# Kernel optimization log

Measured on AMD Instinct MI355X. Metric: run time of the kernel, lower is better.

The kernel has to match this reference:

```python
import jax, jax.numpy as jnp
import numpy as np


def setup_inputs() -> dict:
    key = jax.random.key(0)
    ks = jax.random.split(key, 8)
    B, T, F, H, O = 512, 128, 512, 512, 256
    s = 0.05
    return {
        "states": jax.random.normal(ks[0], (B, T, F), jnp.float32),
        "terminated": jax.random.bernoulli(ks[1], 0.02, (B, T)),
        "h0": jnp.zeros((B, H), jnp.float32),
        "W_ih": jax.random.normal(ks[2], (H, F), jnp.float32) * s,
        "W_hh": jax.random.normal(ks[3], (H, H), jnp.float32) * s,
        "b_ih": jax.random.normal(ks[4], (H,), jnp.float32) * s,
        "b_hh": jax.random.normal(ks[5], (H,), jnp.float32) * s,
        "fc_w": jax.random.normal(ks[6], (O, H), jnp.float32) * s,
        "fc_b": jax.random.normal(ks[7], (O,), jnp.float32) * s,
    }


def reference(states, terminated, h0, W_ih, W_hh, b_ih, b_hh, fc_w, fc_b):
    # states: [B, T, F]; terminated: [B, T] bool; h0: [B, H] (num_layers=1)
    B, T, F = states.shape
    # Precompute the input projection once (big GEMM outside the scan).
    x_proj = jnp.einsum("btf,hf->bth", states, W_ih) + b_ih + b_hh  # [B, T, H]
    x_proj_t = jnp.swapaxes(x_proj, 0, 1)          # [T, B, H]
    term_t = jnp.swapaxes(terminated, 0, 1)        # [T, B]

    def step(h, inp):
        xp, tm = inp                               # xp: [B, H], tm: [B]
        h_new = jnp.tanh(xp + h @ W_hh.T)          # vanilla RNN (tanh) cell
        # Zero hidden state of envs that terminated at this step (applied
        # AFTER emitting the output, matching the torch segment-reset logic).
        h_next = jnp.where(tm[:, None], jnp.zeros_like(h_new), h_new)
        return h_next, h_new

    h_final, outs = jax.lax.scan(step, h0, (x_proj_t, term_t))  # outs: [T, B, H]
    rnn_output = jnp.swapaxes(outs, 0, 1).reshape(B * T, -1)    # [B*T, H]
    logits = rnn_output @ fc_w.T + fc_b                          # [B*T, O]
    return logits, h_final
```

## Files before the change

### kernel.cpp

```cpp
#include <hip/hip_runtime.h>
#include <hip/hip_bf16.h>
#include <hip/hip_fp16.h>


typedef _Float16 half8 __attribute__((ext_vector_type(8)));
typedef _Float16 half4 __attribute__((ext_vector_type(4)));
typedef float f32x4 __attribute__((ext_vector_type(4)));

#define XPW_OFF   0UL
#define WIH_OFF   67108864UL
#define FCW_OFF   67633152UL
#define BIAS_OFF  67895296UL
#define WRESA_OFF 67897344UL
#define WRESL_OFF 68290560UL


#define HB_STRIDE 136

#define LDS_BARRIER()                                              \
    do {                                                           \
        __builtin_amdgcn_sched_barrier(0);                         \
        asm volatile("s_waitcnt lgkmcnt(0)" ::: "memory");         \
        __builtin_amdgcn_s_barrier();                              \
        __builtin_amdgcn_sched_barrier(0);                         \
    } while (0)

__global__ void conv_w(const float* __restrict__ Wih, const float* __restrict__ Whh,
                       const float* __restrict__ fcw, const float* __restrict__ bih,
                       const float* __restrict__ bhh,
                       _Float16* __restrict__ wih_h, _Float16* __restrict__ fcw_h,
                       float* __restrict__ bias2,
                       _Float16* __restrict__ wresA, _Float16* __restrict__ wresL) {
    int idx = blockIdx.x * 256 + threadIdx.x;
    if (idx < 262144) wih_h[idx] = (_Float16)Wih[idx];
    if (idx < 196608) {
        const int i = idx & 7, l = (idx >> 3) & 63, s = (idx >> 9) & 15;
        const int rest = idx >> 13;
        const int w = rest / 3, nt = rest % 3;
        const int row = w * 64 + (l & 15) * 4 + nt;
        wresA[idx] = (_Float16)Whh[(size_t)row * 512 + s * 32 + (l >> 4) * 8 + i];
    }
    if (idx < 65536) {
        const int i = idx & 7, l = (idx >> 3) & 63, s = (idx >> 9) & 15, w = idx >> 13;
        const int row = w * 64 + (l & 15) * 4 + 3;
        wresL[idx] = (_Float16)Whh[(size_t)row * 512 + s * 32 + (l >> 4) * 8 + i];
    }
    if (idx < 131072) fcw_h[idx] = (_Float16)fcw[idx];
    if (idx < 512) bias2[idx] = bih[idx] + bhh[idx];
}

__global__ __launch_bounds__(256) void gemm_xproj(const float* __restrict__ A,
                                                  const _Float16* __restrict__ Bw,
                                                  const float* __restrict__ bias2,
                                                  _Float16* __restrict__ out) {
    __shared__ _Float16 As[128 * 32];
    __shared__ _Float16 Bs[128 * 32];
    __shared__ _Float16 ep[128 * 128];
    const int tid = threadIdx.x;
    const int s_ = blockIdx.x;
    const int z = s_ & 7, k_ = s_ >> 3;
    const int gid = z * 256 + k_;
    const int b = gid >> 2;
    const int cb2 = gid & 3;
    const int lane = tid & 63, w1 = tid >> 6;
    const int wr = (w1 >> 1) * 64, wc = (w1 & 1) * 64;
    const int ln = lane & 15, kg = lane >> 4;

    f32x4 acc[4][4];
#pragma unroll
    for (int m = 0; m < 4; m++)
#pragma unroll
        for (int n = 0; n < 4; n++) acc[m][n] = (f32x4)0.0f;

    const int sr = tid >> 1, sc = (tid & 1) * 16;
    const int brow = cb2 * 128 + sr;

    for (int k0 = 0; k0 < 512; k0 += 32) {
        {
            const float* ga = A + (size_t)(b * 128 + sr) * 512 + k0 + sc;
            float4 f0 = *(const float4*)(ga + 0);
            float4 f1 = *(const float4*)(ga + 4);
            float4 f2 = *(const float4*)(ga + 8);
            float4 f3 = *(const float4*)(ga + 12);
            half8 h0, h1;
            h0[0] = (_Float16)f0.x; h0[1] = (_Float16)f0.y; h0[2] = (_Float16)f0.z; h0[3] = (_Float16)f0.w;
            h0[4] = (_Float16)f1.x; h0[5] = (_Float16)f1.y; h0[6] = (_Float16)f1.z; h0[7] = (_Float16)f1.w;
            h1[0] = (_Float16)f2.x; h1[1] = (_Float16)f2.y; h1[2] = (_Float16)f2.z; h1[3] = (_Float16)f2.w;
            h1[4] = (_Float16)f3.x; h1[5] = (_Float16)f3.y; h1[6] = (_Float16)f3.z; h1[7] = (_Float16)f3.w;
            *(half8*)&As[sr * 32 + sc] = h0;
            *(half8*)&As[sr * 32 + sc + 8] = h1;
        }
        {
            const _Float16* gb = Bw + (size_t)brow * 512 + k0 + sc;
            *(half8*)&Bs[sr * 32 + sc] = *(const half8*)(gb);
            *(half8*)&Bs[sr * 32 + sc + 8] = *(const half8*)(gb + 8);
        }
        __syncthreads();
        half8 af[4], bf[4];
#pragma unroll
        for (int m = 0; m < 4; m++) af[m] = *(const half8*)&As[(wr + m * 16 + ln) * 32 + kg * 8];
#pragma unroll
        for (int n = 0; n < 4; n++) bf[n] = *(const half8*)&Bs[(wc + n * 16 + ln) * 32 + kg * 8];
#pragma unroll
        for (int m = 0; m < 4; m++)
#pragma unroll
            for (int n = 0; n < 4; n++)
                acc[m][n] = __builtin_amdgcn_mfma_f32_16x16x32_f16(af[m], bf[n], acc[m][n], 0, 0, 0);
        __syncthreads();
    }
    float bv[4];
#pragma unroll
    for (int n = 0; n < 4; n++) bv[n] = bias2[cb2 * 128 + wc + n * 16 + ln];
#pragma unroll
    for (int m = 0; m < 4; m++)
#pragma unroll
        for (int q = 0; q < 4; q++) {
            const int t = wr + m * 16 + kg * 4 + q;
#pragma unroll
            for (int n = 0; n < 4; n++)
                ep[t * 128 + wc + n * 16 + ln] = (_Float16)(acc[m][n][q] + bv[n]);
        }
    __syncthreads();
    const int bg = b >> 4, kgs = (b >> 2) & 3, qs = b & 3;
    const size_t obase = (size_t)(bg * 128) * 8192 + (size_t)(cb2 * 2 * 64 + kgs * 16) * 16 + qs * 4;
#pragma unroll
    for (int j = 0; j < 16; j++) {
        const int wid = j * 256 + tid;
        const int t2 = wid >> 5, slb = wid & 31;
        const half4 v = *(const half4*)&ep[t2 * 128 + slb * 4];
        *(half4*)&out[obase + (size_t)t2 * 8192 + (slb >> 4) * 1024 + (slb & 15) * 16] = v;
    }
}

__global__ __launch_bounds__(512, 2) void rnn_scan16(
    const _Float16* __restrict__ xps,
    const _Float16* __restrict__ wresA,
    const _Float16* __restrict__ wresL,
    const int* __restrict__ term,
    const float* __restrict__ h0,
    float* dout) {
    __shared__ __align__(16) _Float16 hb[64 * HB_STRIDE];
    __shared__ __align__(16) _Float16 wl[65536];
    __shared__ unsigned int term_lds[16][4];
    const int tid = threadIdx.x;
    const int bg = blockIdx.x;
    const int R0 = bg * 16;
    const int lane = tid & 63, w = tid >> 6;
    const int ln = lane & 15, kg = lane >> 4;
    _Float16* rnn = (_Float16*)dout;

    half8 wf[48];
    {
        const _Float16* wp = wresA + (size_t)w * 24576 + lane * 8;
#pragma unroll
        for (int f = 0; f < 48; f++) wf[f] = *(const half8*)(wp + (size_t)f * 512);
    }
#pragma unroll
    for (int f = 0; f < 48; f++) asm volatile("" : "+a"(wf[f]));

    for (int u = 0; u < 16; u++) {
        const int o = (u * 512 + tid) * 8;
        *(half8*)&wl[o] = *(const half8*)(wresL + o);
    }
    {
        const int r = tid >> 5, c0 = (tid & 31) * 16;
        const float* gh = h0 + (size_t)(R0 + r) * 512 + c0;
        half8 v0, v1;
#pragma unroll
        for (int i = 0; i < 8; i++) { v0[i] = (_Float16)gh[i]; v1[i] = (_Float16)gh[8 + i]; }
        const int kb = c0 >> 3;
        *(half8*)&hb[kb * HB_STRIDE + r * 8] = v0;
        *(half8*)&hb[(kb + 1) * HB_STRIDE + r * 8] = v1;
    }
    if (tid < 64) {
        const int r = tid >> 2, word = tid & 3;
        unsigned int m = 0;
        for (int b2 = 0; b2 < 32; b2++)
            m |= (term[(R0 + r) * 128 + word * 32 + b2] ? 1u : 0u) << b2;
        term_lds[r][word] = m;
    }
    __syncthreads();

    const _Float16* xpt = xps + (size_t)(bg * 128) * 8192 + tid * 16;
    const _Float16* bl = &wl[(size_t)w * 8192];
    const int cb = w * 64 + ln * 4;
    const int hoff = (cb >> 3) * HB_STRIDE + (cb & 7);
    unsigned int tmask[4];

#pragma unroll 1
    for (int t = 0; t < 128; ++t) {
        if ((t & 31) == 0) {
#pragma unroll
            for (int q = 0; q < 4; q++) tmask[q] = term_lds[kg * 4 + q][t >> 5];
        }
        const half8 xv0 = *(const half8*)(xpt);
        const half8 xv1 = *(const half8*)(xpt + 8);
        xpt += 8192;

        f32x4 acc[4];
#pragma unroll
        for (int n = 0; n < 4; n++) acc[n] = (f32x4)0.0f;

#pragma unroll
        for (int s = 0; s < 16; s++) {
            const half8 a = *(const half8*)&hb[(s * 4 + kg) * HB_STRIDE + ln * 8];
            acc[0] = __builtin_amdgcn_mfma_f32_16x16x32_f16(a, wf[s],      acc[0], 0, 0, 0);
            acc[1] = __builtin_amdgcn_mfma_f32_16x16x32_f16(a, wf[16 + s], acc[1], 0, 0, 0);
            acc[2] = __builtin_amdgcn_mfma_f32_16x16x32_f16(a, wf[32 + s], acc[2], 0, 0, 0);
            const half8 b4 = *(const half8*)(bl + s * 512 + lane * 8);
            acc[3] = __builtin_amdgcn_mfma_f32_16x16x32_f16(a, b4, acc[3], 0, 0, 0);
        }
        LDS_BARRIER();

        half4 hh4[4];
#pragma unroll
        for (int q = 0; q < 4; q++) {
            const bool dead = (tmask[q] >> (t & 31)) & 1;
            half4 v;
#pragma unroll
            for (int nt = 0; nt < 4; nt++) {
                const int u = q * 4 + nt;
                const float xval = (float)(u < 8 ? xv0[u] : xv1[u - 8]);
                const float pre = acc[nt][q] + xval;
                const float e = __expf(2.0f * pre);
                v[nt] = (_Float16)(1.0f - 2.0f * __builtin_amdgcn_rcpf(e + 1.0f));
            }
            hh4[q] = v;
            half4 mv = v;
            if (dead) { mv[0] = (_Float16)0; mv[1] = (_Float16)0; mv[2] = (_Float16)0; mv[3] = (_Float16)0; }
            *(half4*)&hb[hoff + (kg * 4 + q) * 8] = mv;
        }
        LDS_BARRIER();

#pragma unroll
        for (int q = 0; q < 4; q++)
            *(half4*)&rnn[((size_t)(R0 + kg * 4 + q) * 128 + t) * 512 + cb] = hh4[q];
    }

    {
        const int r = tid >> 5, c0 = (tid & 31) * 16;
        const int kb = c0 >> 3;
        half8 v0 = *(const half8*)&hb[kb * HB_STRIDE + r * 8];
        half8 v1 = *(const half8*)&hb[(kb + 1) * HB_STRIDE + r * 8];
        float* gf = dout + (size_t)65536 * 256 + (size_t)(R0 + r) * 512 + c0;
#pragma unroll
        for (int i = 0; i < 8; i++) { gf[i] = (float)v0[i]; gf[8 + i] = (float)v1[i]; }
    }
}

__global__ __launch_bounds__(512) void gemm_logits(const _Float16* Arnn,
                                                   const _Float16* __restrict__ Bw,
                                                   const float* __restrict__ biasv,
                                                   float* out) {
    __shared__ _Float16 As[128 * 32];
    __shared__ _Float16 Bs[256 * 32];
    const int tid = threadIdx.x;
    const int m0 = blockIdx.x * 128;
    const int lane = tid & 63, w = tid >> 6;
    const int wr = (w >> 2) * 64, wc = (w & 3) * 64;
    const int ln = lane & 15, kg = lane >> 4;

    f32x4 acc[4][4];
#pragma unroll
    for (int m = 0; m < 4; m++)
#pragma unroll
        for (int n = 0; n < 4; n++) acc[m][n] = (f32x4)0.0f;

    const int ar = tid >> 2, ac = (tid & 3) * 8;
    const int br = tid >> 1, bc = (tid & 1) * 16;

    for (int k0 = 0; k0 < 512; k0 += 32) {
        *(half8*)&As[ar * 32 + ac] = *(const half8*)(Arnn + (size_t)(m0 + ar) * 512 + k0 + ac);
        {
            const _Float16* gb = Bw + (size_t)br * 512 + k0 + bc;
            *(half8*)&Bs[br * 32 + bc] = *(const half8*)(gb);
            *(half8*)&Bs[br * 32 + bc + 8] = *(const half8*)(gb + 8);
        }
        __syncthreads();
        half8 af[4], bf[4];
#pragma unroll
        for (int m = 0; m < 4; m++) af[m] = *(const half8*)&As[(wr + m * 16 + ln) * 32 + kg * 8];
#pragma unroll
        for (int n = 0; n < 4; n++) bf[n] = *(const half8*)&Bs[(wc + n * 16 + ln) * 32 + kg * 8];
#pragma unroll
        for (int m = 0; m < 4; m++)
#pragma unroll
            for (int n = 0; n < 4; n++)
                acc[m][n] = __builtin_amdgcn_mfma_f32_16x16x32_f16(af[m], bf[n], acc[m][n], 0, 0, 0);
        __syncthreads();
    }
#pragma unroll
    for (int m = 0; m < 4; m++)
#pragma unroll
        for (int n = 0; n < 4; n++) {
            const int col = wc + n * 16 + ln;
            const float bv = biasv[col];
#pragma unroll
            for (int q = 0; q < 4; q++) {
                const int row = m0 + wr + m * 16 + kg * 4 + q;
                out[(size_t)row * 256 + col] = acc[m][n][q] + bv;
            }
        }
}

extern "C" void kernel_launch(void* const* d_in, const int* in_sizes, int n_in,
                              void* d_out, int out_size, void* d_ws, size_t ws_size,
                              hipStream_t stream) {
    const float* states = (const float*)d_in[0];
    const int*   term   = (const int*)d_in[1];
    const float* h0     = (const float*)d_in[2];
    const float* Wih    = (const float*)d_in[3];
    const float* Whh    = (const float*)d_in[4];
    const float* bih    = (const float*)d_in[5];
    const float* bhh    = (const float*)d_in[6];
    const float* fcw    = (const float*)d_in[7];
    const float* fcb    = (const float*)d_in[8];

    char* ws = (char*)d_ws;
    _Float16* xpw   = (_Float16*)(ws + XPW_OFF);
    _Float16* wih_h = (_Float16*)(ws + WIH_OFF);
    _Float16* fcw_h = (_Float16*)(ws + FCW_OFF);
    float*    bias2 = (float*)(ws + BIAS_OFF);
    _Float16* wresA = (_Float16*)(ws + WRESA_OFF);
    _Float16* wresL = (_Float16*)(ws + WRESL_OFF);

    conv_w<<<1024, 256, 0, stream>>>(Wih, Whh, fcw, bih, bhh, wih_h, fcw_h, bias2, wresA, wresL);
    gemm_xproj<<<2048, 256, 0, stream>>>(states, wih_h, bias2, xpw);
    rnn_scan16<<<32, 512, 0, stream>>>(xpw, wresA, wresL, term, h0, (float*)d_out);
    gemm_logits<<<512, 512, 0, stream>>>((const _Float16*)d_out, fcw_h, fcb, (float*)d_out);
}
```

Before: 397.3 us.

## Double-buffer RNN hidden state in LDS to drop one barrier per step

```diff
diff --git a/kernel.cpp b/kernel.cpp
--- a/kernel.cpp
+++ b/kernel.cpp
@@ -14,8 +14,6 @@
 #define WRESA_OFF 67897344UL
 #define WRESL_OFF 68290560UL
 
-
-#define HB_STRIDE 136
 
 #define LDS_BARRIER()                                              \
     do {                                                           \
@@ -132,16 +130,15 @@
     }
 }
 
-__global__ __launch_bounds__(512, 2) void rnn_scan16(
+__global__ __launch_bounds__(512, 2) void rnn_scan17(
     const _Float16* __restrict__ xps,
     const _Float16* __restrict__ wresA,
     const _Float16* __restrict__ wresL,
     const int* __restrict__ term,
     const float* __restrict__ h0,
     float* dout) {
-    __shared__ __align__(16) _Float16 hb[64 * HB_STRIDE];
+    __shared__ __align__(16) _Float16 hb[16384];
     __shared__ __align__(16) _Float16 wl[65536];
-    __shared__ unsigned int term_lds[16][4];
     const int tid = threadIdx.x;
     const int bg = blockIdx.x;
     const int R0 = bg * 16;
@@ -158,6 +155,28 @@
 #pragma unroll
     for (int f = 0; f < 48; f++) asm volatile("" : "+a"(wf[f]));
 
+    unsigned tmr0[4], tmr1[4], tmr2[4], tmr3[4];
+    {
+        unsigned* tw = (unsigned*)wl;
+        if (tid < 64) {
+            const int r = tid >> 2, word = tid & 3;
+            unsigned m = 0;
+            for (int b2 = 0; b2 < 32; b2++)
+                m |= (term[(R0 + r) * 128 + word * 32 + b2] ? 1u : 0u) << b2;
+            tw[tid] = m;
+        }
+        __syncthreads();
+#pragma unroll
+        for (int q = 0; q < 4; q++) {
+            const int r4 = (kg * 4 + q) * 4;
+            tmr0[q] = tw[r4 + 0];
+            tmr1[q] = tw[r4 + 1];
+            tmr2[q] = tw[r4 + 2];
+            tmr3[q] = tw[r4 + 3];
+        }
+        __syncthreads();
+    }
+
     for (int u = 0; u < 16; u++) {
         const int o = (u * 512 + tid) * 8;
         *(half8*)&wl[o] = *(const half8*)(wresL + o);
@@ -169,48 +188,51 @@
 #pragma unroll
         for (int i = 0; i < 8; i++) { v0[i] = (_Float16)gh[i]; v1[i] = (_Float16)gh[8 + i]; }
         const int kb = c0 >> 3;
-        *(half8*)&hb[kb * HB_STRIDE + r * 8] = v0;
-        *(half8*)&hb[(kb + 1) * HB_STRIDE + r * 8] = v1;
-    }
-    if (tid < 64) {
-        const int r = tid >> 2, word = tid & 3;
-        unsigned int m = 0;
-        for (int b2 = 0; b2 < 32; b2++)
-            m |= (term[(R0 + r) * 128 + word * 32 + b2] ? 1u : 0u) << b2;
-        term_lds[r][word] = m;
+        *(half8*)&hb[kb * 128 + ((r ^ (kb & 7)) << 3)] = v0;
+        *(half8*)&hb[(kb + 1) * 128 + ((r ^ ((kb + 1) & 7)) << 3)] = v1;
     }
     __syncthreads();
 
     const _Float16* xpt = xps + (size_t)(bg * 128) * 8192 + tid * 16;
     const _Float16* bl = &wl[(size_t)w * 8192];
     const int cb = w * 64 + ln * 4;
-    const int hoff = (cb >> 3) * HB_STRIDE + (cb & 7);
-    unsigned int tmask[4];
+    const int kbw = cb >> 3;
+    const int A0 = kg * 128 + ((ln ^ kg) << 3);
+    const int A1 = kg * 128 + ((ln ^ (kg + 4)) << 3);
+    int woff[4];
+#pragma unroll
+    for (int q = 0; q < 4; q++)
+        woff[q] = kbw * 128 + ((((kg * 4 + q) ^ (kbw & 7))) << 3) + (cb & 7);
+    unsigned tmask[4];
 
 #pragma unroll 1
     for (int t = 0; t < 128; ++t) {
         if ((t & 31) == 0) {
-#pragma unroll
-            for (int q = 0; q < 4; q++) tmask[q] = term_lds[kg * 4 + q][t >> 5];
+            const int sel = t >> 5;
+#pragma unroll
+            for (int q = 0; q < 4; q++)
+                tmask[q] = sel == 0 ? tmr0[q] : sel == 1 ? tmr1[q] : sel == 2 ? tmr2[q] : tmr3[q];
         }
         const half8 xv0 = *(const half8*)(xpt);
         const half8 xv1 = *(const half8*)(xpt + 8);
         xpt += 8192;
 
+        const _Float16* hr = hb + (t & 1) * 8192;
+        _Float16* hw = hb + ((t & 1) ^ 1) * 8192;
+
         f32x4 acc[4];
 #pragma unroll
         for (int n = 0; n < 4; n++) acc[n] = (f32x4)0.0f;
 
 #pragma unroll
         for (int s = 0; s < 16; s++) {
-            const half8 a = *(const half8*)&hb[(s * 4 + kg) * HB_STRIDE + ln * 8];
+            const half8 a = *(const half8*)&hr[s * 512 + ((s & 1) ? A1 : A0)];
             acc[0] = __builtin_amdgcn_mfma_f32_16x16x32_f16(a, wf[s],      acc[0], 0, 0, 0);
             acc[1] = __builtin_amdgcn_mfma_f32_16x16x32_f16(a, wf[16 + s], acc[1], 0, 0, 0);
             acc[2] = __builtin_amdgcn_mfma_f32_16x16x32_f16(a, wf[32 + s], acc[2], 0, 0, 0);
             const half8 b4 = *(const half8*)(bl + s * 512 + lane * 8);
             acc[3] = __builtin_amdgcn_mfma_f32_16x16x32_f16(a, b4, acc[3], 0, 0, 0);
         }
-        LDS_BARRIER();
 
         half4 hh4[4];
 #pragma unroll
@@ -228,20 +250,21 @@
             hh4[q] = v;
             half4 mv = v;
             if (dead) { mv[0] = (_Float16)0; mv[1] = (_Float16)0; mv[2] = (_Float16)0; mv[3] = (_Float16)0; }
-            *(half4*)&hb[hoff + (kg * 4 + q) * 8] = mv;
-        }
-        LDS_BARRIER();
+            *(half4*)&hw[woff[q]] = mv;
+        }
 
 #pragma unroll
         for (int q = 0; q < 4; q++)
             *(half4*)&rnn[((size_t)(R0 + kg * 4 + q) * 128 + t) * 512 + cb] = hh4[q];
+
+        LDS_BARRIER();
     }
 
     {
         const int r = tid >> 5, c0 = (tid & 31) * 16;
         const int kb = c0 >> 3;
-        half8 v0 = *(const half8*)&hb[kb * HB_STRIDE + r * 8];
-        half8 v1 = *(const half8*)&hb[(kb + 1) * HB_STRIDE + r * 8];
+        half8 v0 = *(const half8*)&hb[kb * 128 + ((r ^ (kb & 7)) << 3)];
+        half8 v1 = *(const half8*)&hb[(kb + 1) * 128 + ((r ^ ((kb + 1) & 7)) << 3)];
         float* gf = dout + (size_t)65536 * 256 + (size_t)(R0 + r) * 512 + c0;
 #pragma unroll
         for (int i = 0; i < 8; i++) { gf[i] = (float)v0[i]; gf[8 + i] = (float)v1[i]; }
@@ -326,6 +349,6 @@
 
     conv_w<<<1024, 256, 0, stream>>>(Wih, Whh, fcw, bih, bhh, wih_h, fcw_h, bias2, wresA, wresL);
     gemm_xproj<<<2048, 256, 0, stream>>>(states, wih_h, bias2, xpw);
-    rnn_scan16<<<32, 512, 0, stream>>>(xpw, wresA, wresL, term, h0, (float*)d_out);
+    rnn_scan17<<<32, 512, 0, stream>>>(xpw, wresA, wresL, term, h0, (float*)d_out);
     gemm_logits<<<512, 512, 0, stream>>>((const _Float16*)d_out, fcw_h, fcb, (float*)d_out);
 }
```

After: 494.8 us. +24.5%, slower.

## Interleave two batch groups per block in RNN scan to overlap MFMA and tanh

Applied to the files above, without the earlier changes.

```diff
diff --git a/kernel.cpp b/kernel.cpp
--- a/kernel.cpp
+++ b/kernel.cpp
@@ -13,6 +13,7 @@
 #define BIAS_OFF  67895296UL
 #define WRESA_OFF 67897344UL
 #define WRESL_OFF 68290560UL
+#define WV_OFF    68413440UL
 
 
 #define HB_STRIDE 136
@@ -30,7 +31,8 @@
                        const float* __restrict__ bhh,
                        _Float16* __restrict__ wih_h, _Float16* __restrict__ fcw_h,
                        float* __restrict__ bias2,
-                       _Float16* __restrict__ wresA, _Float16* __restrict__ wresL) {
+                       _Float16* __restrict__ wresA, _Float16* __restrict__ wresL,
+                       _Float16* __restrict__ wv) {
     int idx = blockIdx.x * 256 + threadIdx.x;
     if (idx < 262144) wih_h[idx] = (_Float16)Wih[idx];
     if (idx < 196608) {
@@ -40,10 +42,16 @@
         const int row = w * 64 + (l & 15) * 4 + nt;
         wresA[idx] = (_Float16)Whh[(size_t)row * 512 + s * 32 + (l >> 4) * 8 + i];
     }
-    if (idx < 65536) {
-        const int i = idx & 7, l = (idx >> 3) & 63, s = (idx >> 9) & 15, w = idx >> 13;
+    if (idx < 61440) {
+        const int i = idx & 7, l = (idx >> 3) & 63, f = idx >> 9;
+        const int w = f / 15, s = f % 15;
         const int row = w * 64 + (l & 15) * 4 + 3;
         wresL[idx] = (_Float16)Whh[(size_t)row * 512 + s * 32 + (l >> 4) * 8 + i];
+    }
+    if (idx < 4096) {
+        const int i = idx & 7, l = (idx >> 3) & 63, w = idx >> 9;
+        const int row = w * 64 + (l & 15) * 4 + 3;
+        wv[idx] = (_Float16)Whh[(size_t)row * 512 + 480 + (l >> 4) * 8 + i];
     }
     if (idx < 131072) fcw_h[idx] = (_Float16)fcw[idx];
     if (idx < 512) bias2[idx] = bih[idx] + bhh[idx];
@@ -132,19 +140,22 @@
     }
 }
 
-__global__ __launch_bounds__(512, 2) void rnn_scan16(
+__global__ __launch_bounds__(512, 2) void rnn_scan19(
     const _Float16* __restrict__ xps,
     const _Float16* __restrict__ wresA,
     const _Float16* __restrict__ wresL,
+    const _Float16* __restrict__ wvsrc,
     const int* __restrict__ term,
     const float* __restrict__ h0,
     float* dout) {
-    __shared__ __align__(16) _Float16 hb[64 * HB_STRIDE];
-    __shared__ __align__(16) _Float16 wl[65536];
-    __shared__ unsigned int term_lds[16][4];
+    __shared__ __align__(16) _Float16 hbA[64 * HB_STRIDE];
+    __shared__ __align__(16) _Float16 hbB[64 * HB_STRIDE];
+    __shared__ __align__(16) _Float16 wl[61440];
+    __shared__ unsigned int term_lds[32][4];
     const int tid = threadIdx.x;
     const int bg = blockIdx.x;
-    const int R0 = bg * 16;
+    const int R0A = bg * 32;
+    const int R0B = bg * 32 + 16;
     const int lane = tid & 63, w = tid >> 6;
     const int ln = lane & 15, kg = lane >> 4;
     _Float16* rnn = (_Float16*)dout;
@@ -158,93 +169,136 @@
 #pragma unroll
     for (int f = 0; f < 48; f++) asm volatile("" : "+a"(wf[f]));
 
-    for (int u = 0; u < 16; u++) {
+    half8 wv = *(const half8*)(wvsrc + (size_t)w * 512 + lane * 8);
+    asm volatile("" : "+v"(wv));
+
+    for (int u = 0; u < 15; u++) {
         const int o = (u * 512 + tid) * 8;
         *(half8*)&wl[o] = *(const half8*)(wresL + o);
     }
     {
         const int r = tid >> 5, c0 = (tid & 31) * 16;
-        const float* gh = h0 + (size_t)(R0 + r) * 512 + c0;
-        half8 v0, v1;
-#pragma unroll
-        for (int i = 0; i < 8; i++) { v0[i] = (_Float16)gh[i]; v1[i] = (_Float16)gh[8 + i]; }
         const int kb = c0 >> 3;
-        *(half8*)&hb[kb * HB_STRIDE + r * 8] = v0;
-        *(half8*)&hb[(kb + 1) * HB_STRIDE + r * 8] = v1;
-    }
-    if (tid < 64) {
+        {
+            const float* gh = h0 + (size_t)(R0A + r) * 512 + c0;
+            half8 v0, v1;
+#pragma unroll
+            for (int i = 0; i < 8; i++) { v0[i] = (_Float16)gh[i]; v1[i] = (_Float16)gh[8 + i]; }
+            *(half8*)&hbA[kb * HB_STRIDE + r * 8] = v0;
+            *(half8*)&hbA[(kb + 1) * HB_STRIDE + r * 8] = v1;
+        }
+        {
+            const float* gh = h0 + (size_t)(R0B + r) * 512 + c0;
+            half8 v0, v1;
+#pragma unroll
+            for (int i = 0; i < 8; i++) { v0[i] = (_Float16)gh[i]; v1[i] = (_Float16)gh[8 + i]; }
+            *(half8*)&hbB[kb * HB_STRIDE + r * 8] = v0;
+            *(half8*)&hbB[(kb + 1) * HB_STRIDE + r * 8] = v1;
+        }
+    }
+    if (tid < 128) {
         const int r = tid >> 2, word = tid & 3;
         unsigned int m = 0;
         for (int b2 = 0; b2 < 32; b2++)
-            m |= (term[(R0 + r) * 128 + word * 32 + b2] ? 1u : 0u) << b2;
+            m |= (term[(R0A + r) * 128 + word * 32 + b2] ? 1u : 0u) << b2;
         term_lds[r][word] = m;
     }
     __syncthreads();
 
-    const _Float16* xpt = xps + (size_t)(bg * 128) * 8192 + tid * 16;
-    const _Float16* bl = &wl[(size_t)w * 8192];
+    const _Float16* xptA = xps + (size_t)(2 * bg * 128) * 8192 + tid * 16;
+    const _Float16* xptB = xptA + (size_t)128 * 8192;
+    const _Float16* bl = &wl[(size_t)w * 7680];
     const int cb = w * 64 + ln * 4;
     const int hoff = (cb >> 3) * HB_STRIDE + (cb & 7);
-    unsigned int tmask[4];
-
-#pragma unroll 1
-    for (int t = 0; t < 128; ++t) {
-        if ((t & 31) == 0) {
-#pragma unroll
-            for (int q = 0; q < 4; q++) tmask[q] = term_lds[kg * 4 + q][t >> 5];
-        }
-        const half8 xv0 = *(const half8*)(xpt);
-        const half8 xv1 = *(const half8*)(xpt + 8);
-        xpt += 8192;
-
-        f32x4 acc[4];
+
+    auto mfma_grp = [&](const _Float16* hx, f32x4* acc) {
 #pragma unroll
         for (int n = 0; n < 4; n++) acc[n] = (f32x4)0.0f;
-
 #pragma unroll
         for (int s = 0; s < 16; s++) {
-            const half8 a = *(const half8*)&hb[(s * 4 + kg) * HB_STRIDE + ln * 8];
+            const half8 a = *(const half8*)&hx[(s * 4 + kg) * HB_STRIDE + ln * 8];
             acc[0] = __builtin_amdgcn_mfma_f32_16x16x32_f16(a, wf[s],      acc[0], 0, 0, 0);
             acc[1] = __builtin_amdgcn_mfma_f32_16x16x32_f16(a, wf[16 + s], acc[1], 0, 0, 0);
             acc[2] = __builtin_amdgcn_mfma_f32_16x16x32_f16(a, wf[32 + s], acc[2], 0, 0, 0);
-            const half8 b4 = *(const half8*)(bl + s * 512 + lane * 8);
+            const half8 b4 = (s < 15) ? *(const half8*)(bl + s * 512 + lane * 8) : wv;
             acc[3] = __builtin_amdgcn_mfma_f32_16x16x32_f16(a, b4, acc[3], 0, 0, 0);
         }
-        LDS_BARRIER();
-
-        half4 hh4[4];
+    };
+    auto finish_grp = [&](f32x4* acc, const half8& x0, const half8& x1,
+                          const unsigned* tm, int t, _Float16* hx, int rbase) {
 #pragma unroll
         for (int q = 0; q < 4; q++) {
-            const bool dead = (tmask[q] >> (t & 31)) & 1;
+            const bool dead = (tm[q] >> (t & 31)) & 1;
             half4 v;
 #pragma unroll
             for (int nt = 0; nt < 4; nt++) {
                 const int u = q * 4 + nt;
-                const float xval = (float)(u < 8 ? xv0[u] : xv1[u - 8]);
+                const float xval = (float)(u < 8 ? x0[u] : x1[u - 8]);
                 const float pre = acc[nt][q] + xval;
                 const float e = __expf(2.0f * pre);
                 v[nt] = (_Float16)(1.0f - 2.0f * __builtin_amdgcn_rcpf(e + 1.0f));
             }
-            hh4[q] = v;
+            *(half4*)&rnn[((size_t)(rbase + kg * 4 + q) * 128 + t) * 512 + cb] = v;
             half4 mv = v;
             if (dead) { mv[0] = (_Float16)0; mv[1] = (_Float16)0; mv[2] = (_Float16)0; mv[3] = (_Float16)0; }
-            *(half4*)&hb[hoff + (kg * 4 + q) * 8] = mv;
-        }
+            *(half4*)&hx[hoff + (kg * 4 + q) * 8] = mv;
+        }
+    };
+
+    half8 xA0 = *(const half8*)(xptA), xA1 = *(const half8*)(xptA + 8);
+    half8 xB0 = *(const half8*)(xptB), xB1 = *(const half8*)(xptB + 8);
+
+    f32x4 accA[4], accB[4];
+    mfma_grp(hbA, accA);
+    LDS_BARRIER();
+
+    unsigned tmA[4], tmB[4];
+
+#pragma unroll 1
+    for (int t = 0; t < 128; ++t) {
+        if ((t & 31) == 0) {
+            const int sel = t >> 5;
+#pragma unroll
+            for (int q = 0; q < 4; q++) {
+                tmA[q] = term_lds[kg * 4 + q][sel];
+                tmB[q] = term_lds[16 + kg * 4 + q][sel];
+            }
+        }
+        const int tn = (t < 127) ? (t + 1) : 127;
+
+        const half8 xBn0 = *(const half8*)(xptB + (size_t)tn * 8192);
+        const half8 xBn1 = *(const half8*)(xptB + (size_t)tn * 8192 + 8);
+        mfma_grp(hbB, accB);
+        finish_grp(accA, xA0, xA1, tmA, t, hbA, R0A);
         LDS_BARRIER();
 
-#pragma unroll
-        for (int q = 0; q < 4; q++)
-            *(half4*)&rnn[((size_t)(R0 + kg * 4 + q) * 128 + t) * 512 + cb] = hh4[q];
+        const half8 xAn0 = *(const half8*)(xptA + (size_t)tn * 8192);
+        const half8 xAn1 = *(const half8*)(xptA + (size_t)tn * 8192 + 8);
+        if (t < 127) mfma_grp(hbA, accA);
+        finish_grp(accB, xB0, xB1, tmB, t, hbB, R0B);
+        LDS_BARRIER();
+
+        xA0 = xAn0; xA1 = xAn1;
+        xB0 = xBn0; xB1 = xBn1;
     }
 
     {
         const int r = tid >> 5, c0 = (tid & 31) * 16;
         const int kb = c0 >> 3;
-        half8 v0 = *(const half8*)&hb[kb * HB_STRIDE + r * 8];
-        half8 v1 = *(const half8*)&hb[(kb + 1) * HB_STRIDE + r * 8];
-        float* gf = dout + (size_t)65536 * 256 + (size_t)(R0 + r) * 512 + c0;
-#pragma unroll
-        for (int i = 0; i < 8; i++) { gf[i] = (float)v0[i]; gf[8 + i] = (float)v1[i]; }
+        {
+            half8 v0 = *(const half8*)&hbA[kb * HB_STRIDE + r * 8];
+            half8 v1 = *(const half8*)&hbA[(kb + 1) * HB_STRIDE + r * 8];
+            float* gf = dout + (size_t)65536 * 256 + (size_t)(R0A + r) * 512 + c0;
+#pragma unroll
+            for (int i = 0; i < 8; i++) { gf[i] = (float)v0[i]; gf[8 + i] = (float)v1[i]; }
+        }
+        {
+            half8 v0 = *(const half8*)&hbB[kb * HB_STRIDE + r * 8];
+            half8 v1 = *(const half8*)&hbB[(kb + 1) * HB_STRIDE + r * 8];
+            float* gf = dout + (size_t)65536 * 256 + (size_t)(R0B + r) * 512 + c0;
+#pragma unroll
+            for (int i = 0; i < 8; i++) { gf[i] = (float)v0[i]; gf[8 + i] = (float)v1[i]; }
+        }
     }
 }
 
@@ -323,9 +377,10 @@
     float*    bias2 = (float*)(ws + BIAS_OFF);
     _Float16* wresA = (_Float16*)(ws + WRESA_OFF);
     _Float16* wresL = (_Float16*)(ws + WRESL_OFF);
-
-    conv_w<<<1024, 256, 0, stream>>>(Wih, Whh, fcw, bih, bhh, wih_h, fcw_h, bias2, wresA, wresL);
+    _Float16* wvb   = (_Float16*)(ws + WV_OFF);
+
+    conv_w<<<1024, 256, 0, stream>>>(Wih, Whh, fcw, bih, bhh, wih_h, fcw_h, bias2, wresA, wresL, wvb);
     gemm_xproj<<<2048, 256, 0, stream>>>(states, wih_h, bias2, xpw);
-    rnn_scan16<<<32, 512, 0, stream>>>(xpw, wresA, wresL, term, h0, (float*)d_out);
+    rnn_scan19<<<16, 512, 0, stream>>>(xpw, wresA, wresL, wvb, term, h0, (float*)d_out);
     gemm_logits<<<512, 512, 0, stream>>>((const _Float16*)d_out, fcw_h, fcb, (float*)d_out);
 }
```

New measurement: 1.285 ms. +223.5%, slower.
